# Performance work log

Hardware: AMD Instinct MI355X
Metric: run time of the kernel (lower is better)

The kernel has to match this reference:

```python
import jax, jax.numpy as jnp
import numpy as np

V, BLK, D, H, L = 32000, 2048, 768, 12, 2
HD = D // H

def _ln(x, g, b, eps=1e-5):
    m = jnp.mean(x, axis=-1, keepdims=True)
    v = jnp.var(x, axis=-1, keepdims=True)
    return (x - m) * jax.lax.rsqrt(v + eps) * g + b

def setup_inputs() -> dict:
    key = jax.random.key(0)
    ks = jax.random.split(key, 16)
    s = 0.02
    return {
        "idx": jax.random.randint(ks[0], (2, 2048), 0, V, dtype=jnp.int32),
        "wte": jax.random.normal(ks[1], (V, D), jnp.float32) * s,
        "wpe": jax.random.normal(ks[2], (BLK, D), jnp.float32) * s,
        "ln1_g": jnp.ones((L, D), jnp.float32),
        "ln1_b": jnp.zeros((L, D), jnp.float32),
        "qkv_w": jax.random.normal(ks[3], (L, 3 * D, D), jnp.float32) * s,
        "qkv_b": jnp.zeros((L, 3 * D), jnp.float32),
        "proj_w": jax.random.normal(ks[4], (L, D, D), jnp.float32) * s,
        "proj_b": jnp.zeros((L, D), jnp.float32),
        "ln2_g": jnp.ones((L, D), jnp.float32),
        "ln2_b": jnp.zeros((L, D), jnp.float32),
        "fc_w": jax.random.normal(ks[5], (L, 4 * D, D), jnp.float32) * s,
        "fc_b": jnp.zeros((L, 4 * D), jnp.float32),
        "fc2_w": jax.random.normal(ks[6], (L, D, 4 * D), jnp.float32) * s,
        "fc2_b": jnp.zeros((L, D), jnp.float32),
        "lnf_g": jnp.ones((D,), jnp.float32),
        "lnf_b": jnp.zeros((D,), jnp.float32),
    }

def reference(idx, wte, wpe, ln1_g, ln1_b, qkv_w, qkv_b, proj_w, proj_b,
              ln2_g, ln2_b, fc_w, fc_b, fc2_w, fc2_b, lnf_g, lnf_b):
    B, T = idx.shape
    x = wte[idx] + wpe[:T][None, :, :]  # [B,T,D]
    causal = jnp.tril(jnp.ones((T, T), dtype=bool))
    scale = 1.0 / np.sqrt(HD)
    for l in range(L):
        h = _ln(x, ln1_g[l], ln1_b[l])
        qkv = h @ qkv_w[l].T + qkv_b[l]               # [B,T,3D]
        q, k, v = jnp.split(qkv, 3, axis=-1)
        q = q.reshape(B, T, H, HD).transpose(0, 2, 1, 3)
        k = k.reshape(B, T, H, HD).transpose(0, 2, 1, 3)
        v = v.reshape(B, T, H, HD).transpose(0, 2, 1, 3)
        att = jnp.einsum('bhqd,bhkd->bhqk', q, k) * scale
        att = jnp.where(causal, att, -jnp.inf)
        att = jax.nn.softmax(att, axis=-1)
        y = jnp.einsum('bhqk,bhkd->bhqd', att, v)
        y = y.transpose(0, 2, 1, 3).reshape(B, T, D)
        x = x + y @ proj_w[l].T + proj_b[l]
        h = _ln(x, ln2_g[l], ln2_b[l])
        h = jax.nn.gelu(h @ fc_w[l].T + fc_b[l], approximate=False)
        x = x + h @ fc2_w[l].T + fc2_b[l]
    x = _ln(x, lnf_g, lnf_b)
    logits = x @ wte.T  # tied lm_head, [B,T,V]
    return logits
```

## Files before the change

kernel.cpp:

```cpp
#include <hip/hip_runtime.h>
#include <hip/hip_bf16.h>
#include <math.h>

#define BB 2
#define TT 2048
#define DD 768
#define HH 12
#define NTOK (BB*TT)
#define VV 32000
#define NL 2

typedef __hip_bfloat16 bf16;
typedef __attribute__((ext_vector_type(8))) short bf16x8;
typedef __attribute__((ext_vector_type(4))) float f32x4;

typedef const __attribute__((address_space(1))) unsigned int* gas_u32;
typedef __attribute__((address_space(3))) unsigned int* las_u32;

__device__ __forceinline__ void gload16(const bf16* g, bf16* l) {
    __builtin_amdgcn_global_load_lds((gas_u32)g, (las_u32)l, 16, 0, 0);
}
__device__ __forceinline__ unsigned short f2bu(float f) {
    bf16 h = __float2bfloat16(f);
    return *reinterpret_cast<unsigned short*>(&h);
}

__global__ __launch_bounds__(256) void cast_all(
    const float* __restrict__ wte, const float* __restrict__ qkv_w,
    const float* __restrict__ proj_w, const float* __restrict__ fc_w,
    const float* __restrict__ fc2_w,
    bf16* __restrict__ o_wte, bf16* __restrict__ o_qkv, bf16* __restrict__ o_prj,
    bf16* __restrict__ o_fc, bf16* __restrict__ o_fc2)
{
    constexpr int N_WTE = VV * DD / 4;
    constexpr int N_QKV = NL * 3 * DD * DD / 4;
    constexpr int N_PRJ = NL * DD * DD / 4;
    constexpr int N_FC  = NL * 4 * DD * DD / 4;
    int g = blockIdx.x * 256 + threadIdx.x;
    const float* s; bf16* d;
    if (g < N_WTE) { s = wte; d = o_wte; }
    else if ((g -= N_WTE) < N_QKV) { s = qkv_w; d = o_qkv; }
    else if ((g -= N_QKV) < N_PRJ) { s = proj_w; d = o_prj; }
    else if ((g -= N_PRJ) < N_FC)  { s = fc_w;  d = o_fc; }
    else { g -= N_FC; s = fc2_w; d = o_fc2; }
    float4 v = reinterpret_cast<const float4*>(s)[g];
    ushort4 r;
    r.x = f2bu(v.x);
    r.y = f2bu(v.y);
    r.z = f2bu(v.z);
    r.w = f2bu(v.w);
    reinterpret_cast<ushort4*>(d)[g] = r;
}

__global__ void embed_k(const int* __restrict__ idx, const float* __restrict__ wte,
                        const float* __restrict__ wpe, float* __restrict__ x) {
    int i = blockIdx.x * 256 + threadIdx.x;
    int n = i / (DD/4), d4 = i - n * (DD/4);
    int tok = idx[n];
    int t = n & (TT - 1);
    float4 a = reinterpret_cast<const float4*>(wte + (size_t)tok * DD)[d4];
    float4 p = reinterpret_cast<const float4*>(wpe + (size_t)t * DD)[d4];
    float4 r; r.x = a.x+p.x; r.y = a.y+p.y; r.z = a.z+p.z; r.w = a.w+p.w;
    reinterpret_cast<float4*>(x)[i] = r;
}

__global__ __launch_bounds__(256) void ln_k(const float* __restrict__ x,
                                            const float* __restrict__ g,
                                            const float* __restrict__ b,
                                            bf16* __restrict__ out) {
    int row = blockIdx.x;
    int tid = threadIdx.x;
    const float* xr = x + (size_t)row * DD;
    float v0 = xr[tid], v1 = xr[tid + 256], v2 = xr[tid + 512];
    float s = v0 + v1 + v2;
    float ss = v0*v0 + v1*v1 + v2*v2;
    #pragma unroll
    for (int d = 1; d < 64; d <<= 1) { s += __shfl_xor(s, d, 64); ss += __shfl_xor(ss, d, 64); }
    __shared__ float sh[8];
    int w = tid >> 6;
    if ((tid & 63) == 0) { sh[w] = s; sh[4 + w] = ss; }
    __syncthreads();
    s  = sh[0] + sh[1] + sh[2] + sh[3];
    ss = sh[4] + sh[5] + sh[6] + sh[7];
    float mean = s * (1.0f / DD);
    float var  = ss * (1.0f / DD) - mean * mean;
    float rstd = rsqrtf(var + 1e-5f);
    bf16* orow = out + (size_t)row * DD;
    orow[tid]       = __float2bfloat16((v0 - mean) * rstd * g[tid]       + b[tid]);
    orow[tid + 256] = __float2bfloat16((v1 - mean) * rstd * g[tid + 256] + b[tid + 256]);
    orow[tid + 512] = __float2bfloat16((v2 - mean) * rstd * g[tid + 512] + b[tid + 512]);
}

template<int EPI, int SWZMODE>
__global__ __launch_bounds__(512, 1) void gemm256(
    const bf16* __restrict__ A, const bf16* __restrict__ W,
    const float* __restrict__ bias, const float* __restrict__ resid,
    void* __restrict__ outp, int O, int K, int nwgx)
{
    __shared__ bf16 smem_bf[65536];
    char* smem = (char*)smem_bf;
    const int tid = threadIdx.x, lane = tid & 63, wid = tid >> 6;
    const int wm = wid >> 2, wn = wid & 3;
    int f = blockIdx.x;
    if (SWZMODE == 1) { int x = f & 7, r = f >> 3; f = x * ((int)gridDim.x >> 3) + r; }
    const int by = f / nwgx;
    const int bx = f - by * nwgx;
    const int rowBase = by * 256, colBase = bx * 256;
    const int rr = lane & 15, s4 = lane >> 4;
    const int swz = (rr >> 1) & 3;
    const int aOff = (wm * 128 + rr) * 64 + ((s4 ^ swz) << 4);
    const int bOff = (wn * 64 + rr) * 64 + ((s4 ^ swz) << 4);
    const int st_r = (wid << 4) + (lane >> 2);
    const int st_j = lane & 3;
    const bf16* Asrc = A + (size_t)rowBase * K;
    const bf16* Wsrc = W + (size_t)colBase * K;
    const int nk = K >> 6;

    auto STAGE = [&](const bf16* src, int mat, int kt, int kk) {
        char* base = smem + ((kt & 1) << 16) + (mat << 15) + (kk << 14);
        #pragma unroll
        for (int L = 0; L < 2; ++L) {
            int r = (L << 7) + st_r;
            int gs = st_j ^ ((r >> 1) & 3);
            gload16(src + (size_t)r * K + (kt << 6) + (kk << 5) + (gs << 3),
                    (bf16*)(base + (L << 13) + (wid << 10)));
        }
    };

    f32x4 acc[8][4];
    #pragma unroll
    for (int m = 0; m < 8; ++m)
        #pragma unroll
        for (int n = 0; n < 4; ++n) acc[m][n] = (f32x4){0.f, 0.f, 0.f, 0.f};

    STAGE(Asrc, 0, 0, 0); STAGE(Wsrc, 1, 0, 0); STAGE(Asrc, 0, 0, 1); STAGE(Wsrc, 1, 0, 1);
    STAGE(Asrc, 0, 1, 0); STAGE(Wsrc, 1, 1, 0); STAGE(Asrc, 0, 1, 1);
    asm volatile("s_waitcnt vmcnt(6)" ::: "memory");
    __builtin_amdgcn_s_barrier();

    bf16x8 af[8], bfr[2];
    for (int kt = 0; kt < nk; ++kt) {
        char* Ab = smem + ((kt & 1) << 16);
        char* Bb = Ab + 32768;
        #pragma unroll
        for (int q = 0; q < 4; ++q) {
            const int kk = q >> 1, nh = q & 1;
            if (nh == 0) {
                #pragma unroll
                for (int m = 0; m < 8; ++m)
                    af[m] = *reinterpret_cast<const bf16x8*>(Ab + (kk << 14) + aOff + (m << 10));
            }
            bfr[0] = *reinterpret_cast<const bf16x8*>(Bb + (kk << 14) + bOff + ((nh * 2 + 0) << 10));
            bfr[1] = *reinterpret_cast<const bf16x8*>(Bb + (kk << 14) + bOff + ((nh * 2 + 1) << 10));
            if (q == 0) { if (kt + 1 < nk) STAGE(Wsrc, 1, kt + 1, 1); }
            else if (q == 1) { if (kt + 2 < nk) STAGE(Asrc, 0, kt + 2, 0); }
            else if (q == 2) { if (kt + 2 < nk) STAGE(Wsrc, 1, kt + 2, 0); }
            else { if (kt + 2 < nk) STAGE(Asrc, 0, kt + 2, 1); }
            __builtin_amdgcn_s_barrier();
            __builtin_amdgcn_s_setprio(1);
            #pragma unroll
            for (int m = 0; m < 8; ++m) {
                acc[m][nh * 2 + 0] = __builtin_amdgcn_mfma_f32_16x16x32_bf16(af[m], bfr[0], acc[m][nh * 2 + 0], 0, 0, 0);
                acc[m][nh * 2 + 1] = __builtin_amdgcn_mfma_f32_16x16x32_bf16(af[m], bfr[1], acc[m][nh * 2 + 1], 0, 0, 0);
            }
            __builtin_amdgcn_s_setprio(0);
            if (q == 3) {
                if (kt == nk - 2) asm volatile("s_waitcnt vmcnt(0)" ::: "memory");
                else              asm volatile("s_waitcnt vmcnt(6)" ::: "memory");
            }
            __builtin_amdgcn_s_barrier();
        }
    }

    if (EPI == 0) {
        float* outf = reinterpret_cast<float*>(outp);
        float* regf = reinterpret_cast<float*>(smem + wid * 4352);
        #pragma unroll
        for (int m = 0; m < 8; ++m) {
            __syncthreads();
            #pragma unroll
            for (int n = 0; n < 4; ++n)
                #pragma unroll
                for (int j2 = 0; j2 < 4; ++j2)
                    regf[(s4 * 4 + j2) * 68 + n * 16 + rr] = acc[m][n][j2];
            __syncthreads();
            #pragma unroll
            for (int i = 0; i < 4; ++i) {
                int fr = wid + i * 8;
                int srcwid = (fr >> 4) * 4 + (lane >> 4);
                f32x4 v = *reinterpret_cast<const f32x4*>(
                    smem + srcwid * 4352 + (fr & 15) * 272 + (lane & 15) * 16);
                int grow = rowBase + (fr >> 4) * 128 + m * 16 + (fr & 15);
                __builtin_nontemporal_store(v,
                    reinterpret_cast<f32x4*>(&outf[(size_t)grow * O + colBase + lane * 4]));
            }
        }
        return;
    }

    #pragma unroll
    for (int m = 0; m < 8; ++m) {
        int row = rowBase + wm * 128 + m * 16 + s4 * 4;
        #pragma unroll
        for (int n = 0; n < 4; ++n) {
            int col = colBase + wn * 64 + n * 16 + rr;
            float bv = bias ? bias[col] : 0.f;
            #pragma unroll
            for (int j2 = 0; j2 < 4; ++j2) {
                float v = acc[m][n][j2] + bv;
                size_t oi = (size_t)(row + j2) * O + col;
                if (EPI == 1) v += resid[oi];
                if (EPI == 3) reinterpret_cast<bf16*>(outp)[oi] = __float2bfloat16(v);
                else          reinterpret_cast<float*>(outp)[oi] = v;
            }
        }
    }
}

template<int EPI, int BN>
__global__ __launch_bounds__(256) void gemm_bt(
    const bf16* __restrict__ A, const bf16* __restrict__ W,
    const float* __restrict__ bias, const float* __restrict__ resid,
    void* __restrict__ outp, int O, int K)
{
    constexpr int NF = BN / 32;
    __shared__ bf16 As[128 * 64];
    __shared__ bf16 Bs[BN * 64];
    const int tid = threadIdx.x;
    const int lane = tid & 63;
    const int w = tid >> 6;
    const int wm = w >> 1, wn = w & 1;
    const int rowBase = blockIdx.y * 128, colBase = blockIdx.x * BN;

    const int rr = lane & 15, s4 = lane >> 4;
    const int st_row = w * 8 + (lane >> 3);
    const int st_col = ((lane & 7) ^ (lane >> 3)) * 8;
    const int r7 = rr & 7;

    f32x4 acc[4][NF];
    #pragma unroll
    for (int m = 0; m < 4; ++m)
        #pragma unroll
        for (int n = 0; n < NF; ++n) acc[m][n] = (f32x4){0.f, 0.f, 0.f, 0.f};

    for (int k0 = 0; k0 < K; k0 += 64) {
        #pragma unroll
        for (int p = 0; p < 4; ++p)
            gload16(&A[(size_t)(rowBase + p * 32 + st_row) * K + k0 + st_col],
                    &As[(p * 32 + w * 8) * 64]);
        #pragma unroll
        for (int p = 0; p < BN / 32; ++p)
            gload16(&W[(size_t)(colBase + p * 32 + st_row) * K + k0 + st_col],
                    &Bs[(p * 32 + w * 8) * 64]);
        __syncthreads();
        #pragma unroll
        for (int kk = 0; kk < 2; ++kk) {
            const int slot = (kk * 4 + s4) ^ r7;
            bf16x8 a[4], b[NF];
            #pragma unroll
            for (int m = 0; m < 4; ++m)
                a[m] = *reinterpret_cast<const bf16x8*>(&As[(wm * 64 + m * 16 + rr) * 64 + slot * 8]);
            #pragma unroll
            for (int n = 0; n < NF; ++n)
                b[n] = *reinterpret_cast<const bf16x8*>(&Bs[(wn * (BN/2) + n * 16 + rr) * 64 + slot * 8]);
            #pragma unroll
            for (int m = 0; m < 4; ++m)
                #pragma unroll
                for (int n = 0; n < NF; ++n)
                    acc[m][n] = __builtin_amdgcn_mfma_f32_16x16x32_bf16(a[m], b[n], acc[m][n], 0, 0, 0);
        }
        __syncthreads();
    }

    #pragma unroll
    for (int m = 0; m < 4; ++m) {
        int row = rowBase + wm * 64 + m * 16 + s4 * 4;
        #pragma unroll
        for (int n = 0; n < NF; ++n) {
            int col = colBase + wn * (BN/2) + n * 16 + rr;
            float bv = bias ? bias[col] : 0.f;
            #pragma unroll
            for (int j2 = 0; j2 < 4; ++j2) {
                float v = acc[m][n][j2] + bv;
                size_t oi = (size_t)(row + j2) * O + col;
                if (EPI == 1) v += resid[oi];
                if (EPI == 2) {
                    v = 0.5f * v * (1.0f + erff(v * 0.70710678118654752f));
                    reinterpret_cast<bf16*>(outp)[oi] = __float2bfloat16(v);
                } else if (EPI == 3) {
                    reinterpret_cast<bf16*>(outp)[oi] = __float2bfloat16(v);
                } else {
                    reinterpret_cast<float*>(outp)[oi] = v;
                }
            }
        }
    }
}

__global__ __launch_bounds__(256, 2) void attn_flash(const bf16* __restrict__ qkvb,
                                                     bf16* __restrict__ ybf)
{
    __shared__ bf16 Qs[128][72];
    __shared__ bf16 Ks[64][72];
    __shared__ bf16 Vt[64][72];

    const int tid = threadIdx.x, lane = tid & 63, w = tid >> 6;
    const int qi = 15 - (blockIdx.x / 24);
    const int bh = blockIdx.x % 24;
    const int b = bh / HH, h = bh % HH;
    const int qbase = qi * 128;
    const int rr = lane & 15, g8 = (lane >> 4) * 8, g4 = (lane >> 4) * 4;

    {
        int seg = tid & 7, jr = tid >> 3;
        #pragma unroll
        for (int p = 0; p < 4; ++p) {
            int q = jr + p * 32;
            *reinterpret_cast<uint4*>(&Qs[q][seg * 8]) =
                *reinterpret_cast<const uint4*>(&qkvb[(size_t)(b*TT + qbase + q) * 2304 + h*64 + seg*8]);
        }
    }
    __syncthreads();

    bf16x8 qf[2][2];
    #pragma unroll
    for (int m = 0; m < 2; ++m)
        #pragma unroll
        for (int c = 0; c < 2; ++c)
            qf[m][c] = *reinterpret_cast<const bf16x8*>(&Qs[w*32 + m*16 + rr][c*32 + g8]);

    float mst[2][4], lst[2][4];
    f32x4 o[2][4];
    #pragma unroll
    for (int m = 0; m < 2; ++m)
        #pragma unroll
        for (int jj = 0; jj < 4; ++jj) { mst[m][jj] = -1e30f; lst[m][jj] = 0.f; }
    #pragma unroll
    for (int m = 0; m < 2; ++m)
        #pragma unroll
        for (int nd = 0; nd < 4; ++nd) o[m][nd] = (f32x4){0.f,0.f,0.f,0.f};

    const int ktmax = 2 * qi + 2;
    for (int kt = 0; kt < ktmax; ++kt) {
        __syncthreads();
        {
            int seg = tid & 7, jr = tid >> 3;
            #pragma unroll
            for (int p = 0; p < 2; ++p) {
                int j = jr + p * 32;
                *reinterpret_cast<uint4*>(&Ks[j][seg * 8]) =
                    *reinterpret_cast<const uint4*>(&qkvb[(size_t)(b*TT + kt*64 + j) * 2304 + DD + h*64 + seg*8]);
            }
            int jv = tid & 31, d0 = (tid >> 5) * 8;
            #pragma unroll
            for (int p = 0; p < 2; ++p) {
                int j = jv + p * 32;
                uint4 raw = *reinterpret_cast<const uint4*>(&qkvb[(size_t)(b*TT + kt*64 + j) * 2304 + 2*DD + h*64 + d0]);
                const bf16* vv = reinterpret_cast<const bf16*>(&raw);
                #pragma unroll
                for (int i2 = 0; i2 < 8; ++i2) Vt[d0 + i2][j] = vv[i2];
            }
        }
        __syncthreads();

        bf16x8 kf[4][2];
        #pragma unroll
        for (int n = 0; n < 4; ++n)
            #pragma unroll
            for (int c = 0; c < 2; ++c)
                kf[n][c] = *reinterpret_cast<const bf16x8*>(&Ks[n*16 + rr][c*32 + g8]);
        f32x4 sacc[2][4];
        #pragma unroll
        for (int m = 0; m < 2; ++m)
            #pragma unroll
            for (int n = 0; n < 4; ++n) sacc[m][n] = (f32x4){0.f,0.f,0.f,0.f};
        #pragma unroll
        for (int m = 0; m < 2; ++m)
            #pragma unroll
            for (int n = 0; n < 4; ++n)
                #pragma unroll
                for (int c = 0; c < 2; ++c)
                    sacc[m][n] = __builtin_amdgcn_mfma_f32_16x16x32_bf16(qf[m][c], kf[n][c], sacc[m][n], 0, 0, 0);

        float corr[2][4];
        #pragma unroll
        for (int m = 0; m < 2; ++m) {
            #pragma unroll
            for (int jj = 0; jj < 4; ++jj) {
                const int qg = qbase + w*32 + m*16 + g4 + jj;
                float pm = -1e30f;
                #pragma unroll
                for (int n = 0; n < 4; ++n) {
                    float v = sacc[m][n][jj] * 0.125f;
                    int jg = kt*64 + n*16 + rr;
                    v = (jg <= qg) ? v : -1e30f;
                    sacc[m][n][jj] = v;
                    pm = fmaxf(pm, v);
                }
                pm = fmaxf(pm, __shfl_xor(pm, 1, 64));
                pm = fmaxf(pm, __shfl_xor(pm, 2, 64));
                pm = fmaxf(pm, __shfl_xor(pm, 4, 64));
                pm = fmaxf(pm, __shfl_xor(pm, 8, 64));
                float nm = fmaxf(mst[m][jj], pm);
                float cv = __expf(mst[m][jj] - nm);
                float r = 0.f;
                #pragma unroll
                for (int n = 0; n < 4; ++n) {
                    float p = __expf(sacc[m][n][jj] - nm);
                    r += p;
                    Qs[w*32 + m*16 + g4 + jj][n*16 + rr] = __float2bfloat16(p);
                }
                r += __shfl_xor(r, 1, 64);
                r += __shfl_xor(r, 2, 64);
                r += __shfl_xor(r, 4, 64);
                r += __shfl_xor(r, 8, 64);
                lst[m][jj] = lst[m][jj] * cv + r;
                mst[m][jj] = nm;
                corr[m][jj] = cv;
            }
        }
        #pragma unroll
        for (int m = 0; m < 2; ++m)
            #pragma unroll
            for (int nd = 0; nd < 4; ++nd)
                #pragma unroll
                for (int jj = 0; jj < 4; ++jj) o[m][nd][jj] *= corr[m][jj];

        __builtin_amdgcn_sched_barrier(0);

        bf16x8 pf[2][2], vf[4][2];
        #pragma unroll
        for (int m = 0; m < 2; ++m)
            #pragma unroll
            for (int c = 0; c < 2; ++c)
                pf[m][c] = *reinterpret_cast<const bf16x8*>(&Qs[w*32 + m*16 + rr][c*32 + g8]);
        #pragma unroll
        for (int nd = 0; nd < 4; ++nd)
            #pragma unroll
            for (int c = 0; c < 2; ++c)
                vf[nd][c] = *reinterpret_cast<const bf16x8*>(&Vt[nd*16 + rr][c*32 + g8]);
        #pragma unroll
        for (int m = 0; m < 2; ++m)
            #pragma unroll
            for (int nd = 0; nd < 4; ++nd)
                #pragma unroll
                for (int c = 0; c < 2; ++c)
                    o[m][nd] = __builtin_amdgcn_mfma_f32_16x16x32_bf16(pf[m][c], vf[nd][c], o[m][nd], 0, 0, 0);
    }

    #pragma unroll
    for (int m = 0; m < 2; ++m) {
        #pragma unroll
        for (int jj = 0; jj < 4; ++jj) {
            const int qg = qbase + w*32 + m*16 + g4 + jj;
            const float inv = 1.0f / lst[m][jj];
            #pragma unroll
            for (int nd = 0; nd < 4; ++nd)
                ybf[(size_t)(b*TT + qg) * DD + h*64 + nd*16 + rr] =
                    __float2bfloat16(o[m][nd][jj] * inv);
        }
    }
}

extern "C" void kernel_launch(void* const* d_in, const int* in_sizes, int n_in,
                              void* d_out, int out_size, void* d_ws, size_t ws_size,
                              hipStream_t stream) {
    const int*   idx    = (const int*)  d_in[0];
    const float* wte    = (const float*)d_in[1];
    const float* wpe    = (const float*)d_in[2];
    const float* ln1_g  = (const float*)d_in[3];
    const float* ln1_b  = (const float*)d_in[4];
    const float* qkv_w  = (const float*)d_in[5];
    const float* qkv_b  = (const float*)d_in[6];
    const float* proj_w = (const float*)d_in[7];
    const float* proj_b = (const float*)d_in[8];
    const float* ln2_g  = (const float*)d_in[9];
    const float* ln2_b  = (const float*)d_in[10];
    const float* fc_w   = (const float*)d_in[11];
    const float* fc_b   = (const float*)d_in[12];
    const float* fc2_w  = (const float*)d_in[13];
    const float* fc2_b  = (const float*)d_in[14];
    const float* lnf_g  = (const float*)d_in[15];
    const float* lnf_b  = (const float*)d_in[16];

    char* ws = (char*)d_ws;
    size_t off = 0;
    auto alloc = [&](size_t bytes) -> void* {
        void* p = ws + off;
        off += (bytes + 255) & ~(size_t)255;
        return p;
    };
    float* x     = (float*)alloc((size_t)NTOK * DD * 4);
    bf16*  qkvb  = (bf16*) alloc((size_t)NTOK * 3 * DD * 2);
    bf16*  lnb   = (bf16*) alloc((size_t)NTOK * DD * 2);
    bf16*  ybf   = (bf16*) alloc((size_t)NTOK * DD * 2);
    bf16*  ffb   = (bf16*) alloc((size_t)NTOK * 4 * DD * 2);
    bf16*  w_qkv = (bf16*) alloc((size_t)NL * 3 * DD * DD * 2);
    bf16*  w_prj = (bf16*) alloc((size_t)NL * DD * DD * 2);
    bf16*  w_fc  = (bf16*) alloc((size_t)NL * 4 * DD * DD * 2);
    bf16*  w_fc2 = (bf16*) alloc((size_t)NL * DD * 4 * DD * 2);
    bf16*  w_wte = (bf16*) alloc((size_t)VV * DD * 2);

    {
        constexpr int totalBlocks = (VV*DD/4 + NL*3*DD*DD/4 + NL*DD*DD/4 +
                                     NL*4*DD*DD/4 + NL*DD*4*DD/4) / 256;
        cast_all<<<dim3(totalBlocks), dim3(256), 0, stream>>>(
            wte, qkv_w, proj_w, fc_w, fc2_w, w_wte, w_qkv, w_prj, w_fc, w_fc2);
    }

    embed_k<<<dim3(NTOK * (DD/4) / 256), dim3(256), 0, stream>>>(idx, wte, wpe, x);

    for (int l = 0; l < NL; ++l) {
        ln_k<<<dim3(NTOK), dim3(256), 0, stream>>>(x, ln1_g + l * DD, ln1_b + l * DD, lnb);
        gemm_bt<3,128><<<dim3(3 * DD / 128, 32), dim3(256), 0, stream>>>(
            lnb, w_qkv + (size_t)l * 3 * DD * DD, qkv_b + l * 3 * DD, nullptr,
            (void*)qkvb, 3 * DD, DD);
        attn_flash<<<dim3(24 * (TT / 128)), dim3(256), 0, stream>>>(qkvb, ybf);
        gemm_bt<1,64><<<dim3(DD / 64, 32), dim3(256), 0, stream>>>(
            ybf, w_prj + (size_t)l * DD * DD, proj_b + l * DD, x,
            (void*)x, DD, DD);
        ln_k<<<dim3(NTOK), dim3(256), 0, stream>>>(x, ln2_g + l * DD, ln2_b + l * DD, lnb);
        gemm_bt<2,128><<<dim3(4 * DD / 128, 32), dim3(256), 0, stream>>>(
            lnb, w_fc + (size_t)l * 4 * DD * DD, fc_b + l * 4 * DD, nullptr,
            (void*)ffb, 4 * DD, DD);
        gemm_bt<1,64><<<dim3(DD / 64, 32), dim3(256), 0, stream>>>(
            ffb, w_fc2 + (size_t)l * DD * 4 * DD, fc2_b + l * DD, x,
            (void*)x, DD, 4 * DD);
    }

    ln_k<<<dim3(NTOK), dim3(256), 0, stream>>>(x, lnf_g, lnf_b, lnb);
    gemm256<0, 1><<<dim3((VV / 256) * (NTOK / 256)), dim3(512), 0, stream>>>(
        lnb, w_wte, nullptr, nullptr, d_out, VV, DD, VV / 256);
}
```

Before: 755.7 us.

## Double-buffer LDS tiles in BN=64 GEMM to overlap global loads with MFMA

For the BN==64 instantiation of the bf16 GEMM, shared-memory tiles are doubled and the next K-tile is issued via global_load_lds before computing on the current one. A partial s_waitcnt vmcnt(6) waits only for the current tile's loads, and raw s_barrier plus s_setprio wrap the compute section. This aims to hide global memory latency behind MFMA work, at the cost of twice the LDS per block, which may reduce occupancy. Other BN variants keep the single-buffer loop.

Result: no change. 753.9 us (median of 2 runs) (-0.2%).

```diff
diff --git a/kernel.cpp b/kernel.cpp
--- a/kernel.cpp
+++ b/kernel.cpp
@@ -224,8 +224,9 @@
     void* __restrict__ outp, int O, int K)
 {
     constexpr int NF = BN / 32;
-    __shared__ bf16 As[128 * 64];
-    __shared__ bf16 Bs[BN * 64];
+    constexpr bool PIPE = (BN == 64);
+    __shared__ bf16 As[(PIPE ? 2 : 1) * 128 * 64];
+    __shared__ bf16 Bs[(PIPE ? 2 : 1) * BN * 64];
     const int tid = threadIdx.x;
     const int lane = tid & 63;
     const int w = tid >> 6;
@@ -243,33 +244,61 @@
         #pragma unroll
         for (int n = 0; n < NF; ++n) acc[m][n] = (f32x4){0.f, 0.f, 0.f, 0.f};
 
-    for (int k0 = 0; k0 < K; k0 += 64) {
+    auto STAGE = [&](int b, int k0) {
         #pragma unroll
         for (int p = 0; p < 4; ++p)
             gload16(&A[(size_t)(rowBase + p * 32 + st_row) * K + k0 + st_col],
-                    &As[(p * 32 + w * 8) * 64]);
+                    &As[b * (128 * 64) + (p * 32 + w * 8) * 64]);
         #pragma unroll
         for (int p = 0; p < BN / 32; ++p)
             gload16(&W[(size_t)(colBase + p * 32 + st_row) * K + k0 + st_col],
-                    &Bs[(p * 32 + w * 8) * 64]);
-        __syncthreads();
+                    &Bs[b * (BN * 64) + (p * 32 + w * 8) * 64]);
+    };
+    auto COMPUTE = [&](int b) {
         #pragma unroll
         for (int kk = 0; kk < 2; ++kk) {
             const int slot = (kk * 4 + s4) ^ r7;
-            bf16x8 a[4], b[NF];
+            bf16x8 a[4], bb[NF];
             #pragma unroll
             for (int m = 0; m < 4; ++m)
-                a[m] = *reinterpret_cast<const bf16x8*>(&As[(wm * 64 + m * 16 + rr) * 64 + slot * 8]);
+                a[m] = *reinterpret_cast<const bf16x8*>(
+                    &As[b * (128 * 64) + (wm * 64 + m * 16 + rr) * 64 + slot * 8]);
             #pragma unroll
             for (int n = 0; n < NF; ++n)
-                b[n] = *reinterpret_cast<const bf16x8*>(&Bs[(wn * (BN/2) + n * 16 + rr) * 64 + slot * 8]);
+                bb[n] = *reinterpret_cast<const bf16x8*>(
+                    &Bs[b * (BN * 64) + (wn * (BN/2) + n * 16 + rr) * 64 + slot * 8]);
             #pragma unroll
             for (int m = 0; m < 4; ++m)
                 #pragma unroll
                 for (int n = 0; n < NF; ++n)
-                    acc[m][n] = __builtin_amdgcn_mfma_f32_16x16x32_bf16(a[m], b[n], acc[m][n], 0, 0, 0);
-        }
-        __syncthreads();
+                    acc[m][n] = __builtin_amdgcn_mfma_f32_16x16x32_bf16(a[m], bb[n], acc[m][n], 0, 0, 0);
+        }
+    };
+
+    if constexpr (PIPE) {
+        const int nk = K >> 6;
+        STAGE(0, 0);
+        for (int kt = 0; kt < nk; ++kt) {
+            const int cur = kt & 1;
+            if (kt + 1 < nk) {
+                STAGE(cur ^ 1, (kt + 1) << 6);
+                asm volatile("s_waitcnt vmcnt(6)" ::: "memory");
+            } else {
+                asm volatile("s_waitcnt vmcnt(0)" ::: "memory");
+            }
+            __builtin_amdgcn_s_barrier();
+            __builtin_amdgcn_s_setprio(1);
+            COMPUTE(cur);
+            __builtin_amdgcn_s_setprio(0);
+            __builtin_amdgcn_s_barrier();
+        }
+    } else {
+        for (int k0 = 0; k0 < K; k0 += 64) {
+            STAGE(0, k0);
+            __syncthreads();
+            COMPUTE(0);
+            __syncthreads();
+        }
     }
 
     #pragma unroll
```
